# Kernel tuning notes

Hardware: AMD Instinct MI355X
Metric: run time of the kernel (lower is better)

The kernel has to match this reference:

```python
import jax, jax.numpy as jnp
import numpy as np


def conv2d(x, w, b):
    # x: (B,C,H,W), w: (O,I,kh,kw), SAME padding, stride 1
    y = jax.lax.conv_general_dilated(x, w, (1, 1), 'SAME',
                                     dimension_numbers=('NCHW', 'OIHW', 'NCHW'))
    return y + b[None, :, None, None]


def setup_inputs() -> dict:
    key = jax.random.key(0)
    ks = jax.random.split(key, 8)
    B, T, C, H, W = 16, 16, 64, 32, 32
    hd = 64  # hidden_dim == input_dim (required by the module's zero-init of h)

    def winit(k, shape):
        fan_in = shape[1] * shape[2] * shape[3]
        return jax.random.normal(k, shape, jnp.float32) / np.float32(np.sqrt(fan_in))

    return {
        'input_tensor': jax.random.normal(ks[0], (B, T, C, H, W), jnp.float32),
        'time_steps': jnp.arange(T, dtype=jnp.float32),
        'mask': jnp.ones((B, T), jnp.float32),
        # ConvGRUCell params
        'w_gates': winit(ks[1], (2 * hd, C + hd, 3, 3)),
        'b_gates': jnp.zeros((2 * hd,), jnp.float32),
        'w_can': winit(ks[2], (hd, C + hd, 3, 3)),
        'b_can': jnp.zeros((hd,), jnp.float32),
        # ODE func params (tanh(conv3x3(x)))
        'w_ode': winit(ks[3], (hd, hd, 3, 3)),
        'b_ode': jnp.zeros((hd,), jnp.float32),
        # transform_z0: conv1x1 -> ReLU -> conv1x1 (z -> 2z)
        'w_t1': winit(ks[4], (hd, hd, 1, 1)),
        'b_t1': jnp.zeros((hd,), jnp.float32),
        'w_t2': winit(ks[5], (2 * hd, hd, 1, 1)),
        'b_t2': jnp.zeros((2 * hd,), jnp.float32),
    }


def reference(input_tensor, time_steps, mask, w_gates, b_gates, w_can, b_can,
              w_ode, b_ode, w_t1, b_t1, w_t2, b_t2):
    B, T, C, H, W = input_tensor.shape
    hd = w_can.shape[0]

    # run_backwards=True: process i = T-1, T-2, ..., 0
    xs = jnp.flip(input_tensor, axis=1).transpose(1, 0, 2, 3, 4)  # (T,B,C,H,W)
    ms = jnp.flip(mask, axis=1).T                                  # (T,B)
    ts_rev = jnp.flip(time_steps)
    # dt_0 = t_last - (t_last + 0.01) = -0.01 ; dt_k = ts[T-k-1] - ts[T-k]
    dts = jnp.concatenate([jnp.full((1,), -0.01, jnp.float32),
                           ts_rev[1:] - ts_rev[:-1]])               # (T,)

    def step(h, inp):
        x, m, dt = inp
        # Euler ODE step: h_ode = h + ode_func(t, h) * dt
        h_ode = h + jnp.tanh(conv2d(h, w_ode, b_ode)) * dt
        # ConvGRU cell
        comb = jnp.concatenate([x, h_ode], axis=1)
        gates = jax.nn.sigmoid(conv2d(comb, w_gates, b_gates))
        reset, update = gates[:, :hd], gates[:, hd:]
        cand = jnp.tanh(conv2d(jnp.concatenate([x, reset * h_ode], axis=1),
                               w_can, b_can))
        h_new = (1.0 - update) * h_ode + update * cand
        mm = m[:, None, None, None]
        h_next = mm * h_new + (1.0 - mm) * h_ode
        return h_next, None

    h0 = jnp.zeros((B, hd, H, W), input_tensor.dtype)
    last_yi, _ = jax.lax.scan(step, h0, (xs, ms, dts))

    z = jax.nn.relu(conv2d(last_yi, w_t1, b_t1))
    z = conv2d(z, w_t2, b_t2)
    mean_z0 = z[:, :hd]
    std_z0 = jnp.abs(z[:, hd:])
    return mean_z0, std_z0
```

## Files before the change

kernel.cpp:

```cpp
#include <hip/hip_runtime.h>
#include <hip/hip_bf16.h>

#define BB 16
#define TT 16

typedef short short8  __attribute__((ext_vector_type(8)));
typedef short short4v __attribute__((ext_vector_type(4)));
typedef float f32x4   __attribute__((ext_vector_type(4)));

__device__ __forceinline__ ushort f2bf(float f) {
    uint u = __float_as_uint(f);
    u += 0x7FFFu + ((u >> 16) & 1u);
    return (ushort)(u >> 16);
}
__device__ __forceinline__ float bf2f(ushort h) { return __uint_as_float(((uint)h) << 16); }
__device__ __forceinline__ float fast_sigmoid(float x) { return 1.0f / (1.0f + __expf(-x)); }
__device__ __forceinline__ float fast_tanh(float x) {
    float e = __expf(2.0f * x);
    return 1.0f - 2.0f / (e + 1.0f);
}

__global__ __launch_bounds__(256)
void pack_all(const float* __restrict__ wg, const float* __restrict__ wc,
              const float* __restrict__ wo, const float* __restrict__ w1,
              const float* __restrict__ w2,
              ushort* __restrict__ wfX, ushort* __restrict__ wfGh,
              ushort* __restrict__ wfCh, ushort* __restrict__ wfO,
              ushort* __restrict__ wf1, ushort* __restrict__ wf2)
{
    const int gi = blockIdx.x * 256 + threadIdx.x;
    const int fi = gi >> 6, lane = gi & 63;
    if (fi >= 528) return;
    const float* src; ushort* dst;
    int CINfull, ci_base, cb_base, CBn, CBT, NT, lf;
    if (fi < 144)      { lf=fi;     src=wg; dst=wfX;  CINfull=128; ci_base=0;  cb_base=0; CBn=8; CBT=12; NT=9; }
    else if (fi < 216) { lf=fi-144; src=wc; dst=wfX;  CINfull=128; ci_base=0;  cb_base=8; CBn=4; CBT=12; NT=9; }
    else if (fi < 360) { lf=fi-216; src=wg; dst=wfGh; CINfull=128; ci_base=64; cb_base=0; CBn=8; CBT=8;  NT=9; }
    else if (fi < 432) { lf=fi-360; src=wc; dst=wfCh; CINfull=128; ci_base=64; cb_base=0; CBn=4; CBT=4;  NT=9; }
    else if (fi < 504) { lf=fi-432; src=wo; dst=wfO;  CINfull=64;  ci_base=0;  cb_base=0; CBn=4; CBT=4;  NT=9; }
    else if (fi < 512) { lf=fi-504; src=w1; dst=wf1;  CINfull=64;  ci_base=0;  cb_base=0; CBn=4; CBT=4;  NT=1; }
    else               { lf=fi-512; src=w2; dst=wf2;  CINfull=64;  ci_base=0;  cb_base=0; CBn=8; CBT=8;  NT=1; }
    const int KCp = 2;
    const int kc = lf % KCp;
    const int cb = (lf / KCp) % CBn;
    const int tap = lf / (KCp * CBn);
    const int co  = cb * 16 + (lane & 15);
    const int ci0 = ci_base + kc * 32 + (lane >> 4) * 8;
    short8 v;
    #pragma unroll
    for (int e = 0; e < 8; ++e)
        v[e] = (short)f2bf(src[((size_t)co * CINfull + ci0 + e) * NT + tap]);
    const size_t fo = ((size_t)(tap * CBT + cb_base + cb)) * KCp + kc;
    *(short8*)(dst + (fo * 64 + lane) * 8) = v;
}

__global__ __launch_bounds__(512)
void conv_x(const float* __restrict__ xall,
            const ushort* __restrict__ wfX,
            const float* __restrict__ b_gates,
            const float* __restrict__ b_can,
            ushort* __restrict__ axc)
{
    extern __shared__ ushort smem[];
    ushort* xb   = smem;
    float*  fraw = (float*)(smem + 13056);
    ushort* outb = smem + 13056;

    const int rt = blockIdx.x, bt = blockIdx.y;
    const int R  = rt * 4;
    const int tid = threadIdx.x;
    const int w = tid >> 6, lane = tid & 63, lr = lane & 15, lg = lane >> 4;
    const float* xs = xall + (size_t)bt * 65536;

    for (int i = tid; i < 3072; i += 512) {
        const int ch = i / 48, rem = i - ch * 48;
        const int tr = rem >> 3, q = rem & 7;
        const int y = R - 1 + tr;
        if ((unsigned)y < 32u)
            *(float4*)(fraw + ch * 199 + tr * 33 + q * 4) =
                *(const float4*)(xs + (size_t)ch * 1024 + y * 32 + q * 4);
    }
    __syncthreads();

    for (int i = tid; i < 1632; i += 512) {
        const int tr = i / 272, rem = i - tr * 272;
        const int hc = rem >> 3, c8 = rem & 7;
        const int y = R - 1 + tr, x = hc - 1;
        short8 v = (short8)0;
        if ((unsigned)y < 32u && (unsigned)x < 32u) {
            #pragma unroll
            for (int e = 0; e < 8; ++e)
                v[e] = (short)f2bf(fraw[(c8 * 8 + e) * 199 + tr * 33 + x]);
        }
        *(short8*)(xb + (tr * 34 + hc) * 64 + ((c8 ^ ((hc + 7) & 7)) << 3)) = v;
    }
    __syncthreads();

    const int cb0 = (w & 3) * 3;
    const int pf0 = (w >> 2) * 4;

    f32x4 acc[3][4];
    #pragma unroll
    for (int i = 0; i < 3; ++i)
        #pragma unroll
        for (int j = 0; j < 4; ++j) acc[i][j] = 0;

    #pragma unroll
    for (int tap = 0; tap < 9; ++tap) {
        const int ky = tap / 3, kx = tap - ky * 3;
        #pragma unroll
        for (int kc = 0; kc < 2; ++kc) {
            short8 a[3];
            #pragma unroll
            for (int i = 0; i < 3; ++i)
                a[i] = *(const short8*)(wfX + (size_t)(((tap * 12 + cb0 + i) * 2 + kc) * 512) + lane * 8);
            #pragma unroll
            for (int j = 0; j < 4; ++j) {
                const int px = (pf0 + j) * 16 + lr;
                const int tr = (px >> 5) + ky, hc = (px & 31) + kx;
                short8 bf = *(const short8*)(xb + (tr * 34 + hc) * 64 + (((kc * 4 + lg) ^ ((hc + 7) & 7)) << 3));
                #pragma unroll
                for (int i = 0; i < 3; ++i)
                    acc[i][j] = __builtin_amdgcn_mfma_f32_16x16x32_bf16(a[i], bf, acc[i][j], 0, 0, 0);
            }
        }
    }
    __syncthreads();

    #pragma unroll
    for (int i = 0; i < 3; ++i) {
        const int co0 = (cb0 + i) * 16 + lg * 4;
        const float* bsrc = (co0 < 128) ? (b_gates + co0) : (b_can + co0 - 128);
        const f32x4 b4 = *(const f32x4*)bsrc;
        #pragma unroll
        for (int j = 0; j < 4; ++j) {
            const int px = (pf0 + j) * 16 + lr;
            short4v s;
            #pragma unroll
            for (int r = 0; r < 4; ++r)
                s[r] = (short)f2bf(acc[i][j][r] + b4[r]);
            *(short4v*)(outb + px * 200 + co0) = s;
        }
    }
    __syncthreads();

    ushort* dst = axc + (((size_t)bt * 1024) + R * 32) * 192;
    for (int i = tid; i < 3072; i += 512) {
        const int px = i / 24, c = i - px * 24;
        *(short8*)(dst + (size_t)px * 192 + c * 8) = *(const short8*)(outb + px * 200 + c * 8);
    }
}

__global__ __launch_bounds__(512, 1)
void fused_step(const ushort* __restrict__ axc,
                const float* __restrict__ h_in,
                const ushort* __restrict__ h_inb,
                float* __restrict__ h_out,
                ushort* __restrict__ h_outb,
                const ushort* __restrict__ wfO,
                const ushort* __restrict__ wfGh,
                const ushort* __restrict__ wfCh,
                const float* __restrict__ b_ode,
                const float* __restrict__ tsteps,
                const float* __restrict__ mask,
                int t)
{
    extern __shared__ ushort smem[];
    float*  smemf = (float*)smem;
    ushort* hbuf  = smem;
    ushort* obuf  = smem + 17408;
    ushort* rhbuf = smem;
    float*  ubuf  = smemf + 4352;
    float*  hode  = smemf + 15232;

    const int l  = blockIdx.x;
    const int rt = 2 * (l & 7) + ((l >> 3) & 1);
    const int b  = l >> 4;
    const int R  = rt * 2;
    const int tid = threadIdx.x;
    const int w = tid >> 6, lane = tid & 63, lr = lane & 15, lg = lane >> 4;
    const int bti = b * TT + (TT - 1 - t);

    const ushort* hbb = h_inb + (size_t)b * 1026 * 64;
    const float*  hb  = h_in  + (size_t)b * 65536;
    const ushort* axb = axc + (size_t)bti * 1024 * 192;

    short4v gxr[2][4], cxr[2];
    {
        const int cq = w & 3, ph = w >> 2;
        #pragma unroll
        for (int i = 0; i < 2; ++i) {
            const int cog0 = (2 * cq + i) * 16 + lg * 4;
            #pragma unroll
            for (int j = 0; j < 4; ++j) {
                const int f = 4 * ph + j;
                const int y = R - 1 + (f >> 1);
                const int c = (f & 1) * 16 + lr;
                short4v g = (short4v)0;
                if ((unsigned)y < 32u)
                    g = *(const short4v*)(axb + ((size_t)(y * 32 + c)) * 192 + cog0);
                gxr[i][j] = g;
            }
        }
        const int cf = w & 3, ph2 = w >> 2;
        const int co0 = cf * 16 + lg * 4;
        #pragma unroll
        for (int j = 0; j < 2; ++j) {
            const int c = j * 16 + lr;
            const int pix = (R + (ph2 & 1)) * 32 + c;
            cxr[j] = *(const short4v*)(axb + (size_t)pix * 192 + 128 + co0);
        }
    }

    for (int i = tid; i < 2176; i += 512) {
        const int tr = i / 272, rem = i - tr * 272;
        const int hc = rem >> 3;
        const int y  = R - 3 + tr;
        short8 v = (short8)0;
        if (t != 0 && (unsigned)y < 32u && hc != 0 && hc != 33)
            v = *(const short8*)(hbb + ((size_t)(y * 32 + hc)) * 64 + (rem & 7) * 8);
        *(short8*)(hbuf + (size_t)i * 8) = v;
    }
    for (int i = tid; i < 1632; i += 512) {
        const int tr = i / 272, rem = i - tr * 272;
        const int hc = rem >> 3;
        const int y  = R - 2 + tr;
        if (hc == 0 || hc == 33 || (unsigned)y >= 32u)
            *(short8*)(obuf + (size_t)i * 8) = (short8)0;
    }
    __syncthreads();

    {
        const int cb0 = (w & 1) * 2;
        const int pxg = w >> 1;
        f32x4 accA[2][3];
        #pragma unroll
        for (int i = 0; i < 2; ++i)
            #pragma unroll
            for (int j = 0; j < 3; ++j) accA[i][j] = 0;

        #pragma unroll
        for (int tap = 0; tap < 9; ++tap) {
            const int ky = tap / 3, kx = tap - ky * 3;
            #pragma unroll
            for (int kc = 0; kc < 2; ++kc) {
                short8 a0 = *(const short8*)(wfO + (size_t)(((tap * 4 + cb0 + 0) * 2 + kc) * 512) + lane * 8);
                short8 a1 = *(const short8*)(wfO + (size_t)(((tap * 4 + cb0 + 1) * 2 + kc) * 512) + lane * 8);
                #pragma unroll
                for (int j = 0; j < 3; ++j) {
                    const int p  = (3 * pxg + j) * 16 + lr;
                    const int tr = (p >> 5) + ky, hc = (p & 31) + kx;
                    short8 bf = *(const short8*)(hbuf + (tr * 34 + hc) * 64 + ((((kc << 2) + lg) ^ ((hc + 7) & 7)) << 3));
                    accA[0][j] = __builtin_amdgcn_mfma_f32_16x16x32_bf16(a0, bf, accA[0][j], 0, 0, 0);
                    accA[1][j] = __builtin_amdgcn_mfma_f32_16x16x32_bf16(a1, bf, accA[1][j], 0, 0, 0);
                }
            }
        }
        const float dt = (t == 0) ? -0.01f : (tsteps[TT - 1 - t] - tsteps[TT - t]);
        #pragma unroll
        for (int i = 0; i < 2; ++i) {
            #pragma unroll
            for (int j = 0; j < 3; ++j) {
                const int co0 = (cb0 + i) * 16 + lg * 4;
                const int p = (3 * pxg + j) * 16 + lr;
                const int orow = p >> 5, c = p & 31;
                const int y = R - 2 + orow;
                if ((unsigned)y < 32u) {
                    const int key = (((co0 >> 3) ^ (c & 7)) << 3) + (co0 & 7);
                    f32x4 h4;
                    if ((unsigned)(y - R) < 2u) {
                        if (t == 0) {
                            h4 = 0;
                        } else {
                            h4 = *(const f32x4*)(hb + ((size_t)(y * 32 + c)) * 64 + co0);
                        }
                    } else {
                        short4v hv = *(const short4v*)(hbuf + ((orow + 1) * 34 + c + 1) * 64 + key);
                        #pragma unroll
                        for (int r = 0; r < 4; ++r) h4[r] = bf2f((ushort)hv[r]);
                    }
                    const f32x4 b4 = *(const f32x4*)(b_ode + co0);
                    f32x4 ho;
                    #pragma unroll
                    for (int r = 0; r < 4; ++r)
                        ho[r] = h4[r] + fast_tanh(accA[i][j][r] + b4[r]) * dt;
                    short4v s;
                    #pragma unroll
                    for (int r = 0; r < 4; ++r) s[r] = (short)f2bf(ho[r]);
                    *(short4v*)(obuf + (orow * 34 + c + 1) * 64 + key) = s;
                    if ((unsigned)(y - R) < 2u)
                        *(f32x4*)(hode + ((y - R) * 32 + c) * 64 + (((co0 >> 2) ^ (c & 15)) << 2)) = ho;
                }
            }
        }
    }
    __syncthreads();

    for (int i = tid; i < 1088; i += 512) {
        const int tr = i / 272, rem = i - tr * 272;
        const int hc = rem >> 3;
        const int y  = R - 1 + tr;
        if (hc == 0 || hc == 33 || (unsigned)y >= 32u)
            *(short8*)(rhbuf + (size_t)i * 8) = (short8)0;
    }

    {
        const int cq = w & 3, ph = w >> 2;
        f32x4 accB[2][4];
        #pragma unroll
        for (int i = 0; i < 2; ++i)
            #pragma unroll
            for (int j = 0; j < 4; ++j) {
                f32x4 g;
                #pragma unroll
                for (int r = 0; r < 4; ++r) g[r] = bf2f((ushort)gxr[i][j][r]);
                accB[i][j] = g;
            }

        #pragma unroll
        for (int tap = 0; tap < 9; ++tap) {
            const int ky = tap / 3, kx = tap - ky * 3;
            #pragma unroll
            for (int kc = 0; kc < 2; ++kc) {
                short8 a0 = *(const short8*)(wfGh + (size_t)(((tap * 8 + 2 * cq + 0) * 2 + kc) * 512) + lane * 8);
                short8 a1 = *(const short8*)(wfGh + (size_t)(((tap * 8 + 2 * cq + 1) * 2 + kc) * 512) + lane * 8);
                #pragma unroll
                for (int j = 0; j < 4; ++j) {
                    const int f  = 4 * ph + j;
                    const int tr = (f >> 1) + ky;
                    const int hc = (f & 1) * 16 + lr + kx;
                    short8 bf = *(const short8*)(obuf + (tr * 34 + hc) * 64 + ((((kc << 2) + lg) ^ ((hc + 7) & 7)) << 3));
                    accB[0][j] = __builtin_amdgcn_mfma_f32_16x16x32_bf16(a0, bf, accB[0][j], 0, 0, 0);
                    accB[1][j] = __builtin_amdgcn_mfma_f32_16x16x32_bf16(a1, bf, accB[1][j], 0, 0, 0);
                }
            }
        }
        #pragma unroll
        for (int i = 0; i < 2; ++i) {
            const int cog = (2 * cq + i) * 16 + lg * 4;
            #pragma unroll
            for (int j = 0; j < 4; ++j) {
                const int f = 4 * ph + j;
                const int y = R - 1 + (f >> 1);
                const int c = (f & 1) * 16 + lr;
                if (cq < 2) {
                    if ((unsigned)y < 32u) {
                        const int tro = (f >> 1) + 1;
                        const int key = (((cog >> 3) ^ (c & 7)) << 3) + (cog & 7);
                        short4v ho4 = *(const short4v*)(obuf + (tro * 34 + c + 1) * 64 + key);
                        short4v s;
                        #pragma unroll
                        for (int r = 0; r < 4; ++r)
                            s[r] = (short)f2bf(fast_sigmoid(accB[i][j][r]) * bf2f((ushort)ho4[r]));
                        *(short4v*)(rhbuf + ((f >> 1) * 34 + c + 1) * 64 + key) = s;
                    }
                } else if ((unsigned)(y - R) < 2u) {
                    const int cu = cog - 64;
                    f32x4 u;
                    #pragma unroll
                    for (int r = 0; r < 4; ++r)
                        u[r] = fast_sigmoid(accB[i][j][r]);
                    *(f32x4*)(ubuf + ((y - R) * 32 + c) * 64 + (((cu >> 2) ^ (c & 15)) << 2)) = u;
                }
            }
        }
    }
    __syncthreads();

    {
        const int cf = w & 3, ph2 = w >> 2;
        const int co0 = cf * 16 + lg * 4;
        f32x4 accC[2];
        #pragma unroll
        for (int j = 0; j < 2; ++j) {
            f32x4 g;
            #pragma unroll
            for (int r = 0; r < 4; ++r) g[r] = bf2f((ushort)cxr[j][r]);
            accC[j] = g;
        }

        #pragma unroll
        for (int tap = 0; tap < 9; ++tap) {
            const int ky = tap / 3, kx = tap - ky * 3;
            #pragma unroll
            for (int kc = 0; kc < 2; ++kc) {
                short8 a = *(const short8*)(wfCh + (size_t)(((tap * 4 + cf) * 2 + kc) * 512) + lane * 8);
                #pragma unroll
                for (int j = 0; j < 2; ++j) {
                    const int tr = ph2 + ky;
                    const int hc = j * 16 + lr + kx;
                    short8 bf = *(const short8*)(rhbuf + (tr * 34 + hc) * 64 + ((((kc << 2) + lg) ^ ((hc + 7) & 7)) << 3));
                    accC[j] = __builtin_amdgcn_mfma_f32_16x16x32_bf16(a, bf, accC[j], 0, 0, 0);
                }
            }
        }
        const float m = mask[b * TT + (TT - 1 - t)];
        const int y = R + ph2;
        #pragma unroll
        for (int j = 0; j < 2; ++j) {
            const int c = j * 16 + lr;
            const int pi = ph2 * 32 + c;
            const int sw = ((co0 >> 2) ^ (c & 15)) << 2;
            const f32x4 ho = *(const f32x4*)(hode + pi * 64 + sw);
            const f32x4 u  = *(const f32x4*)(ubuf + pi * 64 + sw);
            f32x4 o;
            short4v s;
            #pragma unroll
            for (int r = 0; r < 4; ++r) {
                const float cand = fast_tanh(accC[j][r]);
                o[r] = ho[r] + m * u[r] * (cand - ho[r]);
                s[r] = (short)f2bf(o[r]);
            }
            const int pix = y * 32 + c;
            *(f32x4*)(h_out + (size_t)b * 65536 + (size_t)pix * 64 + co0) = o;
            *(short4v*)(h_outb + ((size_t)b * 1026 + 1 + pix) * 64
                        + (((co0 >> 3) ^ (c & 7)) << 3) + (co0 & 7)) = s;
        }
    }
}

__global__ __launch_bounds__(256)
void head_mfma(const float* __restrict__ h,
               const ushort* __restrict__ w1f, const float* __restrict__ b1,
               const ushort* __restrict__ w2f, const float* __restrict__ b2,
               float* __restrict__ outp)
{
    __shared__ ushort hlds[64 * 64];
    __shared__ ushort zlds[64 * 64];
    const int blk = blockIdx.x, b = blk >> 4, pixb = (blk & 15) * 64;
    const int tid = threadIdx.x, wv = tid >> 6, lane = tid & 63, lr = lane & 15, lg = lane >> 4;
    const float* hb = h + ((size_t)b * 1024 + pixb) * 64;

    for (int idx = tid; idx < 64 * 8; idx += 256) {
        const int c = idx & 7, px = idx >> 3;
        const float* p = hb + (size_t)px * 64 + c * 8;
        short8 v;
        #pragma unroll
        for (int e = 0; e < 8; ++e) v[e] = (short)f2bf(p[e]);
        *(short8*)(hlds + px * 64 + ((c ^ (px & 7)) << 3)) = v;
    }
    __syncthreads();

    f32x4 acc1[4]; acc1[0]=0; acc1[1]=0; acc1[2]=0; acc1[3]=0;
    #pragma unroll
    for (int kc = 0; kc < 2; ++kc) {
        short8 a = *(const short8*)(w1f + (((size_t)wv * 2 + kc) * 64 + lane) * 8);
        #pragma unroll
        for (int p = 0; p < 4; ++p) {
            const int hp = p * 16 + lr;
            short8 bf = *(const short8*)(hlds + hp * 64 + (((kc * 4 + lg) ^ (hp & 7)) << 3));
            acc1[p] = __builtin_amdgcn_mfma_f32_16x16x32_bf16(a, bf, acc1[p], 0, 0, 0);
        }
    }
    {
        const int co0 = wv * 16 + lg * 4;
        const f32x4 b4 = *(const f32x4*)(b1 + co0);
        #pragma unroll
        for (int p = 0; p < 4; ++p) {
            const int px = p * 16 + lr;
            short4v s;
            #pragma unroll
            for (int r = 0; r < 4; ++r)
                s[r] = (short)f2bf(fmaxf(acc1[p][r] + b4[r], 0.0f));
            *(short4v*)(zlds + px * 64 + (((co0 >> 3) ^ (px & 7)) << 3) + (co0 & 7)) = s;
        }
    }
    __syncthreads();

    f32x4 acc2[2][4];
    #pragma unroll
    for (int gi = 0; gi < 2; ++gi)
        #pragma unroll
        for (int p = 0; p < 4; ++p) acc2[gi][p] = 0;
    #pragma unroll
    for (int kc = 0; kc < 2; ++kc) {
        short8 a0 = *(const short8*)(w2f + ((((size_t)wv * 2 + 0) * 2 + kc) * 64 + lane) * 8);
        short8 a1 = *(const short8*)(w2f + ((((size_t)wv * 2 + 1) * 2 + kc) * 64 + lane) * 8);
        #pragma unroll
        for (int p = 0; p < 4; ++p) {
            const int hp = p * 16 + lr;
            short8 bf = *(const short8*)(zlds + hp * 64 + (((kc * 4 + lg) ^ (hp & 7)) << 3));
            acc2[0][p] = __builtin_amdgcn_mfma_f32_16x16x32_bf16(a0, bf, acc2[0][p], 0, 0, 0);
            acc2[1][p] = __builtin_amdgcn_mfma_f32_16x16x32_bf16(a1, bf, acc2[1][p], 0, 0, 0);
        }
    }
    #pragma unroll
    for (int gi = 0; gi < 2; ++gi) {
        const int co0 = wv * 32 + gi * 16 + lg * 4;
        const f32x4 b4 = *(const f32x4*)(b2 + co0);
        #pragma unroll
        for (int p = 0; p < 4; ++p) {
            const int px = pixb + p * 16 + lr;
            #pragma unroll
            for (int r = 0; r < 4; ++r) {
                const int co = co0 + r;
                const float v = acc2[gi][p][r] + b4[r];
                if (co < 64)
                    outp[((size_t)b * 64 + co) * 1024 + px] = v;
                else
                    outp[(size_t)BB * 64 * 1024 + ((size_t)b * 64 + (co - 64)) * 1024 + px] = fabsf(v);
            }
        }
    }
}

extern "C" void kernel_launch(void* const* d_in, const int* in_sizes, int n_in,
                              void* d_out, int out_size, void* d_ws, size_t ws_size,
                              hipStream_t stream)
{
    const float* xall    = (const float*)d_in[0];
    const float* tsteps  = (const float*)d_in[1];
    const float* mask    = (const float*)d_in[2];
    const float* w_gates = (const float*)d_in[3];
    const float* b_gates = (const float*)d_in[4];
    const float* w_can   = (const float*)d_in[5];
    const float* b_can   = (const float*)d_in[6];
    const float* w_ode   = (const float*)d_in[7];
    const float* b_ode   = (const float*)d_in[8];
    const float* w_t1    = (const float*)d_in[9];
    const float* b_t1    = (const float*)d_in[10];
    const float* w_t2    = (const float*)d_in[11];
    const float* b_t2    = (const float*)d_in[12];
    float* out = (float*)d_out;

    float*  h0   = (float*)d_ws;
    float*  h1   = h0 + (size_t)BB * 65536;
    ushort* h0b  = (ushort*)(h1 + (size_t)BB * 65536);
    ushort* h1b  = h0b + (size_t)BB * 1026 * 64;
    ushort* axc  = h1b + (size_t)BB * 1026 * 64;
    ushort* wfX  = axc + (size_t)256 * 1024 * 192;
    ushort* wfGh = wfX  + (size_t)216 * 512;
    ushort* wfCh = wfGh + (size_t)144 * 512;
    ushort* wfO  = wfCh + (size_t)72 * 512;
    ushort* wf1  = wfO  + (size_t)72 * 512;
    ushort* wf2  = wf1  + (size_t)8 * 512;

    pack_all<<<dim3(132), 256, 0, stream>>>(w_gates, w_can, w_ode, w_t1, w_t2,
                                            wfX, wfGh, wfCh, wfO, wf1, wf2);

    hipFuncSetAttribute(reinterpret_cast<const void*>(conv_x),
                        hipFuncAttributeMaxDynamicSharedMemorySize, 77056);
    conv_x<<<dim3(8, 256), 512, 77056, stream>>>(xall, wfX, b_gates, b_can, axc);

    hipFuncSetAttribute(reinterpret_cast<const void*>(fused_step),
                        hipFuncAttributeMaxDynamicSharedMemorySize, 77312);

    for (int t = 0; t < TT; ++t) {
        const float*  hin   = (t & 1) ? h1  : h0;
        float*        hout  = (t & 1) ? h0  : h1;
        const ushort* hinb  = (t & 1) ? h1b : h0b;
        ushort*       houtb = (t & 1) ? h0b : h1b;
        fused_step<<<dim3(256), 512, 77312, stream>>>(axc, hin, hinb, hout, houtb,
                                                      wfO, wfGh, wfCh,
                                                      b_ode, tsteps, mask, t);
    }
    head_mfma<<<dim3(256), 256, 0, stream>>>(h0, wf1, b_t1, wf2, b_t2, out);
}
```

Measured before the change: 396.6 us.

## Fuse head into last recurrent step and streamline conv_x staging

The 1x1-conv head (conv1x1, ReLU, conv1x1, abs) now runs inside the final fused_step launch using the new hidden state already in LDS, which removes the separate head kernel and the final h store/reload. conv_x drops its fp32 staging buffer and converts to bf16 directly into the swizzled LDS tile, which cuts shared memory so more blocks fit per CU. The output copy now uses 4-element stores with a padded stride. This adds branching to the step kernel and scattered 2-byte LDS writes in conv_x.

```diff
diff --git a/kernel.cpp b/kernel.cpp
--- a/kernel.cpp
+++ b/kernel.cpp
@@ -54,7 +54,7 @@
     *(short8*)(dst + (fo * 64 + lane) * 8) = v;
 }
 
-__global__ __launch_bounds__(512)
+__global__ __launch_bounds__(512, 6)
 void conv_x(const float* __restrict__ xall,
             const ushort* __restrict__ wfX,
             const float* __restrict__ b_gates,
@@ -63,8 +63,7 @@
 {
     extern __shared__ ushort smem[];
     ushort* xb   = smem;
-    float*  fraw = (float*)(smem + 13056);
-    ushort* outb = smem + 13056;
+    ushort* outb = smem;
 
     const int rt = blockIdx.x, bt = blockIdx.y;
     const int R  = rt * 4;
@@ -72,27 +71,27 @@
     const int w = tid >> 6, lane = tid & 63, lr = lane & 15, lg = lane >> 4;
     const float* xs = xall + (size_t)bt * 65536;
 
+    for (int i = tid; i < 1632; i += 512) {
+        const int tr = i / 272, rem = i - tr * 272;
+        const int hc = rem >> 3;
+        const int y  = R - 1 + tr;
+        if (hc == 0 || hc == 33 || (unsigned)y >= 32u)
+            *(short8*)(xb + (size_t)i * 8) = (short8)0;
+    }
     for (int i = tid; i < 3072; i += 512) {
         const int ch = i / 48, rem = i - ch * 48;
         const int tr = rem >> 3, q = rem & 7;
         const int y = R - 1 + tr;
-        if ((unsigned)y < 32u)
-            *(float4*)(fraw + ch * 199 + tr * 33 + q * 4) =
-                *(const float4*)(xs + (size_t)ch * 1024 + y * 32 + q * 4);
-    }
-    __syncthreads();
-
-    for (int i = tid; i < 1632; i += 512) {
-        const int tr = i / 272, rem = i - tr * 272;
-        const int hc = rem >> 3, c8 = rem & 7;
-        const int y = R - 1 + tr, x = hc - 1;
-        short8 v = (short8)0;
-        if ((unsigned)y < 32u && (unsigned)x < 32u) {
-            #pragma unroll
-            for (int e = 0; e < 8; ++e)
-                v[e] = (short)f2bf(fraw[(c8 * 8 + e) * 199 + tr * 33 + x]);
-        }
-        *(short8*)(xb + (tr * 34 + hc) * 64 + ((c8 ^ ((hc + 7) & 7)) << 3)) = v;
+        if ((unsigned)y < 32u) {
+            float4 f = *(const float4*)(xs + (size_t)ch * 1024 + y * 32 + q * 4);
+            const float* fp = (const float*)&f;
+            const int c8 = ch >> 3, e = ch & 7;
+            #pragma unroll
+            for (int sub = 0; sub < 4; ++sub) {
+                const int hc = q * 4 + sub + 1;
+                xb[(tr * 34 + hc) * 64 + ((c8 ^ ((hc + 7) & 7)) << 3) + e] = f2bf(fp[sub]);
+            }
+        }
     }
     __syncthreads();
 
@@ -139,15 +138,15 @@
             #pragma unroll
             for (int r = 0; r < 4; ++r)
                 s[r] = (short)f2bf(acc[i][j][r] + b4[r]);
-            *(short4v*)(outb + px * 200 + co0) = s;
+            *(short4v*)(outb + px * 204 + co0) = s;
         }
     }
     __syncthreads();
 
     ushort* dst = axc + (((size_t)bt * 1024) + R * 32) * 192;
-    for (int i = tid; i < 3072; i += 512) {
-        const int px = i / 24, c = i - px * 24;
-        *(short8*)(dst + (size_t)px * 192 + c * 8) = *(const short8*)(outb + px * 200 + c * 8);
+    for (int i = tid; i < 6144; i += 512) {
+        const int px = i / 48, c4 = i - px * 48;
+        *(short4v*)(dst + (size_t)px * 192 + c4 * 4) = *(const short4v*)(outb + px * 204 + c4 * 4);
     }
 }
 
@@ -161,6 +160,9 @@
                 const ushort* __restrict__ wfGh,
                 const ushort* __restrict__ wfCh,
                 const float* __restrict__ b_ode,
+                const ushort* __restrict__ wf1, const float* __restrict__ b_t1,
+                const ushort* __restrict__ wf2, const float* __restrict__ b_t2,
+                float* __restrict__ outp,
                 const float* __restrict__ tsteps,
                 const float* __restrict__ mask,
                 int t)
@@ -172,6 +174,8 @@
     ushort* rhbuf = smem;
     float*  ubuf  = smemf + 4352;
     float*  hode  = smemf + 15232;
+    ushort* hnew  = smem;
+    ushort* zlds  = smem + 8704;
 
     const int l  = blockIdx.x;
     const int rt = 2 * (l & 7) + ((l >> 3) & 1);
@@ -269,11 +273,8 @@
                     const int key = (((co0 >> 3) ^ (c & 7)) << 3) + (co0 & 7);
                     f32x4 h4;
                     if ((unsigned)(y - R) < 2u) {
-                        if (t == 0) {
-                            h4 = 0;
-                        } else {
-                            h4 = *(const f32x4*)(hb + ((size_t)(y * 32 + c)) * 64 + co0);
-                        }
+                        if (t == 0) { h4 = 0; }
+                        else { h4 = *(const f32x4*)(hb + ((size_t)(y * 32 + c)) * 64 + co0); }
                     } else {
                         short4v hv = *(const short4v*)(hbuf + ((orow + 1) * 34 + c + 1) * 64 + key);
                         #pragma unroll
@@ -396,6 +397,7 @@
         }
         const float m = mask[b * TT + (TT - 1 - t)];
         const int y = R + ph2;
+        short4v hsv[2];
         #pragma unroll
         for (int j = 0; j < 2; ++j) {
             const int c = j * 16 + lr;
@@ -411,94 +413,81 @@
                 o[r] = ho[r] + m * u[r] * (cand - ho[r]);
                 s[r] = (short)f2bf(o[r]);
             }
-            const int pix = y * 32 + c;
-            *(f32x4*)(h_out + (size_t)b * 65536 + (size_t)pix * 64 + co0) = o;
-            *(short4v*)(h_outb + ((size_t)b * 1026 + 1 + pix) * 64
-                        + (((co0 >> 3) ^ (c & 7)) << 3) + (co0 & 7)) = s;
-        }
-    }
-}
-
-__global__ __launch_bounds__(256)
-void head_mfma(const float* __restrict__ h,
-               const ushort* __restrict__ w1f, const float* __restrict__ b1,
-               const ushort* __restrict__ w2f, const float* __restrict__ b2,
-               float* __restrict__ outp)
-{
-    __shared__ ushort hlds[64 * 64];
-    __shared__ ushort zlds[64 * 64];
-    const int blk = blockIdx.x, b = blk >> 4, pixb = (blk & 15) * 64;
-    const int tid = threadIdx.x, wv = tid >> 6, lane = tid & 63, lr = lane & 15, lg = lane >> 4;
-    const float* hb = h + ((size_t)b * 1024 + pixb) * 64;
-
-    for (int idx = tid; idx < 64 * 8; idx += 256) {
-        const int c = idx & 7, px = idx >> 3;
-        const float* p = hb + (size_t)px * 64 + c * 8;
-        short8 v;
-        #pragma unroll
-        for (int e = 0; e < 8; ++e) v[e] = (short)f2bf(p[e]);
-        *(short8*)(hlds + px * 64 + ((c ^ (px & 7)) << 3)) = v;
-    }
-    __syncthreads();
-
-    f32x4 acc1[4]; acc1[0]=0; acc1[1]=0; acc1[2]=0; acc1[3]=0;
-    #pragma unroll
-    for (int kc = 0; kc < 2; ++kc) {
-        short8 a = *(const short8*)(w1f + (((size_t)wv * 2 + kc) * 64 + lane) * 8);
-        #pragma unroll
-        for (int p = 0; p < 4; ++p) {
-            const int hp = p * 16 + lr;
-            short8 bf = *(const short8*)(hlds + hp * 64 + (((kc * 4 + lg) ^ (hp & 7)) << 3));
-            acc1[p] = __builtin_amdgcn_mfma_f32_16x16x32_bf16(a, bf, acc1[p], 0, 0, 0);
-        }
-    }
-    {
-        const int co0 = wv * 16 + lg * 4;
-        const f32x4 b4 = *(const f32x4*)(b1 + co0);
-        #pragma unroll
-        for (int p = 0; p < 4; ++p) {
-            const int px = p * 16 + lr;
-            short4v s;
-            #pragma unroll
-            for (int r = 0; r < 4; ++r)
-                s[r] = (short)f2bf(fmaxf(acc1[p][r] + b4[r], 0.0f));
-            *(short4v*)(zlds + px * 64 + (((co0 >> 3) ^ (px & 7)) << 3) + (co0 & 7)) = s;
-        }
-    }
-    __syncthreads();
-
-    f32x4 acc2[2][4];
-    #pragma unroll
-    for (int gi = 0; gi < 2; ++gi)
-        #pragma unroll
-        for (int p = 0; p < 4; ++p) acc2[gi][p] = 0;
-    #pragma unroll
-    for (int kc = 0; kc < 2; ++kc) {
-        short8 a0 = *(const short8*)(w2f + ((((size_t)wv * 2 + 0) * 2 + kc) * 64 + lane) * 8);
-        short8 a1 = *(const short8*)(w2f + ((((size_t)wv * 2 + 1) * 2 + kc) * 64 + lane) * 8);
-        #pragma unroll
-        for (int p = 0; p < 4; ++p) {
-            const int hp = p * 16 + lr;
-            short8 bf = *(const short8*)(zlds + hp * 64 + (((kc * 4 + lg) ^ (hp & 7)) << 3));
-            acc2[0][p] = __builtin_amdgcn_mfma_f32_16x16x32_bf16(a0, bf, acc2[0][p], 0, 0, 0);
-            acc2[1][p] = __builtin_amdgcn_mfma_f32_16x16x32_bf16(a1, bf, acc2[1][p], 0, 0, 0);
-        }
-    }
-    #pragma unroll
-    for (int gi = 0; gi < 2; ++gi) {
-        const int co0 = wv * 32 + gi * 16 + lg * 4;
-        const f32x4 b4 = *(const f32x4*)(b2 + co0);
-        #pragma unroll
-        for (int p = 0; p < 4; ++p) {
-            const int px = pixb + p * 16 + lr;
-            #pragma unroll
-            for (int r = 0; r < 4; ++r) {
-                const int co = co0 + r;
-                const float v = acc2[gi][p][r] + b4[r];
-                if (co < 64)
-                    outp[((size_t)b * 64 + co) * 1024 + px] = v;
-                else
-                    outp[(size_t)BB * 64 * 1024 + ((size_t)b * 64 + (co - 64)) * 1024 + px] = fabsf(v);
+            hsv[j] = s;
+            if (t != TT - 1) {
+                const int pix = y * 32 + c;
+                *(f32x4*)(h_out + (size_t)b * 65536 + (size_t)pix * 64 + co0) = o;
+                *(short4v*)(h_outb + ((size_t)b * 1026 + 1 + pix) * 64
+                            + (((co0 >> 3) ^ (c & 7)) << 3) + (co0 & 7)) = s;
+            }
+        }
+
+        if (t == TT - 1) {
+            __syncthreads();
+            #pragma unroll
+            for (int j = 0; j < 2; ++j) {
+                const int c = j * 16 + lr;
+                const int pl = ph2 * 32 + c;
+                *(short4v*)(hnew + pl * 64 + (((co0 >> 3) ^ (pl & 7)) << 3) + (co0 & 7)) = hsv[j];
+            }
+            __syncthreads();
+
+            {
+                const int cb = w & 3, pxh = w >> 2;
+                f32x4 acc1[2]; acc1[0] = 0; acc1[1] = 0;
+                #pragma unroll
+                for (int kc = 0; kc < 2; ++kc) {
+                    short8 a = *(const short8*)(wf1 + (((size_t)cb * 2 + kc) * 64 + lane) * 8);
+                    #pragma unroll
+                    for (int jj = 0; jj < 2; ++jj) {
+                        const int hp = (pxh * 2 + jj) * 16 + lr;
+                        short8 bf = *(const short8*)(hnew + hp * 64 + (((kc * 4 + lg) ^ (hp & 7)) << 3));
+                        acc1[jj] = __builtin_amdgcn_mfma_f32_16x16x32_bf16(a, bf, acc1[jj], 0, 0, 0);
+                    }
+                }
+                const int zco = cb * 16 + lg * 4;
+                const f32x4 bz = *(const f32x4*)(b_t1 + zco);
+                #pragma unroll
+                for (int jj = 0; jj < 2; ++jj) {
+                    const int px = (pxh * 2 + jj) * 16 + lr;
+                    short4v s;
+                    #pragma unroll
+                    for (int r = 0; r < 4; ++r)
+                        s[r] = (short)f2bf(fmaxf(acc1[jj][r] + bz[r], 0.0f));
+                    *(short4v*)(zlds + px * 64 + (((zco >> 3) ^ (px & 7)) << 3) + (zco & 7)) = s;
+                }
+            }
+            __syncthreads();
+
+            {
+                f32x4 acc2[4];
+                #pragma unroll
+                for (int pf = 0; pf < 4; ++pf) acc2[pf] = 0;
+                #pragma unroll
+                for (int kc = 0; kc < 2; ++kc) {
+                    short8 a = *(const short8*)(wf2 + (((size_t)w * 2 + kc) * 64 + lane) * 8);
+                    #pragma unroll
+                    for (int pf = 0; pf < 4; ++pf) {
+                        const int hp = pf * 16 + lr;
+                        short8 bf = *(const short8*)(zlds + hp * 64 + (((kc * 4 + lg) ^ (hp & 7)) << 3));
+                        acc2[pf] = __builtin_amdgcn_mfma_f32_16x16x32_bf16(a, bf, acc2[pf], 0, 0, 0);
+                    }
+                }
+                const int oco0 = w * 16 + lg * 4;
+                const f32x4 b4 = *(const f32x4*)(b_t2 + oco0);
+                #pragma unroll
+                for (int pf = 0; pf < 4; ++pf) {
+                    const int pix = R * 32 + pf * 16 + lr;
+                    #pragma unroll
+                    for (int r = 0; r < 4; ++r) {
+                        const int co = oco0 + r;
+                        const float v = acc2[pf][r] + b4[r];
+                        if (co < 64)
+                            outp[((size_t)b * 64 + co) * 1024 + pix] = v;
+                        else
+                            outp[(size_t)BB * 64 * 1024 + ((size_t)b * 64 + (co - 64)) * 1024 + pix] = fabsf(v);
+                    }
+                }
             }
         }
     }
@@ -539,8 +528,8 @@
                                             wfX, wfGh, wfCh, wfO, wf1, wf2);
 
     hipFuncSetAttribute(reinterpret_cast<const void*>(conv_x),
-                        hipFuncAttributeMaxDynamicSharedMemorySize, 77056);
-    conv_x<<<dim3(8, 256), 512, 77056, stream>>>(xall, wfX, b_gates, b_can, axc);
+                        hipFuncAttributeMaxDynamicSharedMemorySize, 52224);
+    conv_x<<<dim3(8, 256), 512, 52224, stream>>>(xall, wfX, b_gates, b_can, axc);
 
     hipFuncSetAttribute(reinterpret_cast<const void*>(fused_step),
                         hipFuncAttributeMaxDynamicSharedMemorySize, 77312);
@@ -551,8 +540,8 @@
         const ushort* hinb  = (t & 1) ? h1b : h0b;
         ushort*       houtb = (t & 1) ? h0b : h1b;
         fused_step<<<dim3(256), 512, 77312, stream>>>(axc, hin, hinb, hout, houtb,
-                                                      wfO, wfGh, wfCh,
-                                                      b_ode, tsteps, mask, t);
-    }
-    head_mfma<<<dim3(256), 256, 0, stream>>>(h0, wf1, b_t1, wf2, b_t2, out);
+                                                      wfO, wfGh, wfCh, b_ode,
+                                                      wf1, b_t1, wf2, b_t2, out,
+                                                      tsteps, mask, t);
+    }
 }
```

Result: slower. 643.0 us (+62.1%).
